# Kernel optimization log

Hardware: AMD Instinct MI355X
Metric: run time of the kernel (lower is better)

Reference implementation:

```python
import jax, jax.numpy as jnp
import numpy as np

MC = 16384
IND_T = 96
N_MAT = 4
N_STRIKES = 21


def _init_linear(key, fan_in, fan_out, prefix=()):
    k1, k2 = jax.random.split(key)
    lim = 1.0 / np.sqrt(fan_in)
    W = jax.random.uniform(k1, prefix + (fan_in, fan_out), minval=-lim, maxval=lim, dtype=jnp.float32)
    b = jax.random.uniform(k2, prefix + (fan_out,), minval=-lim, maxval=lim, dtype=jnp.float32)
    return W, b


def setup_inputs() -> dict:
    key = jax.random.key(0)
    ks = jax.random.split(key, 14)
    z = jax.random.normal(ks[0], (MC, IND_T), dtype=jnp.float32)
    zz = jax.random.normal(ks[1], (MC, IND_T), dtype=jnp.float32)
    timegrid = jnp.arange(IND_T + 1, dtype=jnp.float32) / 365.0  # daily grid
    maturities = jnp.array([24, 48, 72, 96], dtype=jnp.int32)    # in days
    strikes = jnp.linspace(0.8, 1.2, N_STRIKES, dtype=jnp.float32)
    sv_W1, sv_b1 = _init_linear(ks[2], 3, 100)
    sv_W2, sv_b2 = _init_linear(ks[3], 100, 100)
    sv_W3, sv_b3 = _init_linear(ks[4], 100, 1)
    vh_W1, vh_b1 = _init_linear(ks[5], 2, 20, (N_MAT,))
    vh_W2, vh_b2 = _init_linear(ks[6], 20, N_STRIKES, (N_MAT,))
    vd_W1, vd_b1 = _init_linear(ks[7], 1, 20)
    vd_W2, vd_b2 = _init_linear(ks[8], 20, 1)
    vv_W1, vv_b1 = _init_linear(ks[9], 1, 20)
    vv_W2, vv_b2 = _init_linear(ks[10], 20, 1)
    v0 = jax.random.uniform(ks[11], (1,), dtype=jnp.float32) * 0.1
    rho = jnp.ones((1,), dtype=jnp.float32) * -2.0
    return dict(S0=jnp.float32(1.0), rate=jnp.float32(0.05), z=z, zz=zz,
                timegrid=timegrid, strikes=strikes, v0=v0, rho=rho,
                sv_W1=sv_W1, sv_b1=sv_b1, sv_W2=sv_W2, sv_b2=sv_b2, sv_W3=sv_W3, sv_b3=sv_b3,
                vh_W1=vh_W1, vh_b1=vh_b1, vh_W2=vh_W2, vh_b2=vh_b2,
                vd_W1=vd_W1, vd_b1=vd_b1, vd_W2=vd_W2, vd_b2=vd_b2,
                vv_W1=vv_W1, vv_b1=vv_b1, vv_W2=vv_W2, vv_b2=vv_b2,
                maturities=maturities)


def reference(S0, rate, z, zz, timegrid, strikes, v0, rho,
              sv_W1, sv_b1, sv_W2, sv_b2, sv_W3, sv_b3,
              vh_W1, vh_b1, vh_W2, vh_b2,
              vd_W1, vd_b1, vd_W2, vd_b2,
              vv_W1, vv_b1, vv_W2, vv_b2,
              maturities):
    sg = jax.lax.stop_gradient
    mc = z.shape[0]
    n_mat = vh_W1.shape[0]
    n_strikes = strikes.shape[0]

    def s_vol(x):  # [MC,3] -> [MC,1], softplus output
        h1 = jax.nn.relu(x @ sv_W1 + sv_b1)
        h2 = jax.nn.relu(h1 @ sv_W2 + sv_b2)
        return jax.nn.softplus(h2 @ sv_W3 + sv_b3)

    def v_drift(v):  # [MC,1] -> [MC,1]
        return jax.nn.relu(v @ vd_W1 + vd_b1) @ vd_W2 + vd_b2

    def v_vol(v):  # [MC,1] -> [MC,1], softplus output
        return jax.nn.softplus(jax.nn.relu(v @ vv_W1 + vv_b1) @ vv_W2 + vv_b2)

    def vanilla_hedge_all(x):  # [MC,2] -> [MC, n_strikes, n_mat] (one net per maturity)
        h1 = jax.nn.relu(jnp.einsum('mi,kio->kmo', x, vh_W1) + vh_b1[:, None, :])
        out = jax.nn.softplus(jnp.einsum('kmo,koj->kmj', h1, vh_W2) + vh_b2[:, None, :])
        return jnp.transpose(out, (1, 2, 0))

    rho_t = jnp.tanh(rho)[0]
    days = jnp.round(timegrid * 365.0).astype(jnp.int32)       # [IND_T+1]
    le = days[1:, None] <= maturities[None, :]                  # [IND_T, n_mat]
    idx_net = jnp.argmax(le, axis=1)                            # first live maturity per step
    is_mat = jnp.any(days[1:, None] == maturities[None, :], axis=1)
    mat_idx = jnp.arange(n_mat)

    Slog0 = jnp.log(jnp.full((mc, 1), S0, dtype=jnp.float32))
    V0 = jnp.full((mc, 1), 1.0, dtype=jnp.float32) * jax.nn.sigmoid(v0)[0] * 0.5
    cv0 = jnp.zeros((mc, n_strikes, n_mat), dtype=jnp.float32)
    pv0 = jnp.zeros((n_mat, n_strikes), dtype=jnp.float32)

    xs = (z.T[:, :, None], zz.T[:, :, None], timegrid[:-1], timegrid[1:], idx_net, is_mat)

    def step(carry, x):
        Slog_old, V_old, cv, pv_h, pv_var = carry
        z_i, zz_i, t0, t1, idx, im = x
        h = t1 - t0
        sqh = jnp.sqrt(h)
        dW = sqh * z_i                                          # [MC,1]
        dB = rho_t * dW + jnp.sqrt(1.0 - rho_t ** 2) * sqh * zz_i
        ones_t = jnp.full((mc, 1), 1.0, dtype=jnp.float32) * t0
        pd = s_vol(jnp.concatenate([ones_t, Slog_old, V_old], axis=1))  # price diffusion
        cv_fwd = vanilla_hedge_all(jnp.concatenate([ones_t, sg(Slog_old)], axis=1))
        V_new = V_old + v_drift(V_old) * h + v_vol(V_old) * dB
        drift = rate - 0.5 * pd ** 2
        diff = pd * dW
        drift_c = 1.0 + jnp.abs(sg(drift)) * sqh                # tamed Euler
        diff_c = 1.0 + jnp.abs(sg(pd)) * sqh
        Slog_new = Slog_old + drift * h / drift_c + diff / diff_c
        S_new = jnp.exp(Slog_new)
        S_old = jnp.exp(Slog_old)
        dS = jnp.exp(-rate * t1) * S_new - jnp.exp(-rate * t0) * S_old  # [MC,1]
        mask = (mat_idx >= idx).astype(cv.dtype)                # live maturities only
        cv = cv + mask[None, None, :] * cv_fwd * sg(dS)[:, :, None]
        # hedged vanilla (call) prices collected at maturity steps
        payoff = jnp.exp(-rate * t1) * jnp.maximum(S_new - strikes[None, :], 0.0)
        price = payoff - cv[:, :, idx]                          # [MC, n_strikes]
        pv = jnp.mean(price, axis=0)
        pvar = jnp.var(price, axis=0, ddof=1)
        sel = (mat_idx == idx)[:, None] & im
        pv_h = jnp.where(sel, pv[None, :], pv_h)
        pv_var = jnp.where(sel, pvar[None, :], pv_var)
        return (Slog_new, V_new, cv, pv_h, pv_var), None

    (_, _, _, pv_h, pv_var), _ = jax.lax.scan(step, (Slog0, V0, cv0, pv0, pv0), xs)
    return jnp.stack([pv_h, pv_var])  # [2, n_mat, n_strikes]
```

## Files before the change

kernel.cpp:

```cpp
#include <hip/hip_runtime.h>
#include <hip/hip_bf16.h>
#include <math.h>


#define MC      16384
#define NSTEP   96
#define BLOCK   512
#define NGROUP  512
#define NPAIR   84

typedef short bf16x8 __attribute__((ext_vector_type(8)));
typedef float f32x4  __attribute__((ext_vector_type(4)));

union U8 { uint4 u; bf16x8 v; };
union BF2U { __hip_bfloat162 b; unsigned u; };

__device__ __forceinline__ unsigned bf16rne(float x) {
    unsigned u = __float_as_uint(x);
    return (u + 0x7FFFu + ((u >> 16) & 1u)) >> 16;
}
__device__ __forceinline__ unsigned pk2(float lo, float hi) {
    BF2U t; t.b = __float22bfloat162_rn(make_float2(lo, hi));
    return t.u;
}
__device__ __forceinline__ float sp(float x) {
    return fmaxf(x, 0.f) + __logf(1.f + __expf(-fabsf(x)));
}

__global__ __launch_bounds__(BLOCK, 4)
void lsv_sim(const float* __restrict__ S0p,   const float* __restrict__ ratep,
             const float* __restrict__ z,     const float* __restrict__ zzg,
             const float* __restrict__ strikesg,
             const float* __restrict__ v0p,   const float* __restrict__ rhop,
             const float* __restrict__ svW1,  const float* __restrict__ svb1,
             const float* __restrict__ svW2,  const float* __restrict__ svb2,
             const float* __restrict__ svW3,  const float* __restrict__ svb3,
             const float* __restrict__ vhW1,  const float* __restrict__ vhb1,
             const float* __restrict__ vhW2,  const float* __restrict__ vhb2,
             const float* __restrict__ vdW1,  const float* __restrict__ vdb1,
             const float* __restrict__ vdW2,  const float* __restrict__ vdb2,
             const float* __restrict__ vvW1,  const float* __restrict__ vvb1,
             const float* __restrict__ vvW2,  const float* __restrict__ vvb2,
             const int*   __restrict__ mats,
             float* __restrict__ psum, float* __restrict__ psq)
{
    __shared__ __align__(16) unsigned short H1c[16 * 32 * 8];
    __shared__ __align__(16) float W1f[16 * 32];
    __shared__ __align__(16) float WH1f[16 * 32];
    __shared__ __align__(16) float B2T[128], W3T[128];
    __shared__ __align__(16) float RED[32 * 4];
    __shared__ float VDl[32], VVl[32];
    __shared__ float PSs[2][32], PSq[2][32];
    __shared__ __align__(16) float VW[128];
    __shared__ __align__(16) float4 STEP[NSTEP];
    __shared__ float D1T[NSTEP];
    __shared__ int   ITAB[NSTEP];
    __shared__ float ZT[32][97], ZZT[32][97];
    __shared__ float SLOG[32], VST[32], SST[32], SLOGP[32], DSP[32];
    __shared__ __align__(16) float CW1[2][128];
    __shared__ __align__(16) float CH[2][128];

    const int tid  = threadIdx.x;
    const int lane = tid & 63;
    const int w    = __builtin_amdgcn_readfirstlane(tid >> 6);
    const int quad = lane >> 4;
    const int col  = lane & 15;
    const int lp   = lane & 31;

    const int pt = w & 1;
    const int jg = w >> 1;
    const int hm = w >> 1;

    {
        const size_t gbase = (size_t)blockIdx.x * 32 * NSTEP;
        for (int e = tid; e < 32 * NSTEP; e += BLOCK) {
            const int p = e / NSTEP, ii = e - p * NSTEP;
            ZT[p][ii]  = z  [gbase + e];
            ZZT[p][ii] = zzg[gbase + e];
        }
    }
    for (int e = tid; e < 128; e += BLOCK) {
        float v = 0.f;
        if      (e < 20)             v = vdW1[e];
        else if (e < 40)             v = vdb1[e - 20];
        else if (e < 60)             v = vdW2[e - 40];
        else if (e >= 64 && e < 84)  v = vvW1[e - 64];
        else if (e >= 84 && e < 104) v = vvb1[e - 84];
        else if (e >= 104 && e < 124)v = vvW2[e - 104];
        else if (e == 124)           v = vdb2[0];
        else if (e == 125)           v = vvb2[0];
        VW[e] = v;
        B2T[e] = (e < 100) ? svb2[e] : 0.f;
        W3T[e] = (e < 100) ? svW3[e] : 0.f;
    }
    for (int e = tid; e < 512; e += BLOCK) {
        const int kc2 = e >> 5, r5 = e & 31, grp = r5 >> 3, kk = kc2 * 8 + (r5 & 7);
        float v = 0.f;
        if (kk < 100) v = (grp == 0) ? svW1[kk] : (grp == 1) ? svW1[100 + kk]
                        : (grp == 2) ? svW1[200 + kk] : svb1[kk];
        W1f[e] = v;
    }
    for (int e = tid; e < 512; e += BLOCK) {
        const int hq = e >> 5, r5 = e & 31, grp = r5 >> 3;
        const int hmm = hq >> 2, qq = hq & 3;
        const int j = qq * 8 + (r5 & 7);
        float v = 0.f;
        if (j < 20 && grp < 3)
            v = (grp == 0) ? vhW1[hmm * 40 + j] : (grp == 1) ? vhW1[hmm * 40 + 20 + j]
                                                : vhb1[hmm * 20 + j];
        WH1f[e] = v;
    }

    const float rate  = ratep[0];
    const float S0    = S0p[0];
    const float rho_t = tanhf(rhop[0]);
    const float srho  = sqrtf(1.f - rho_t * rho_t);
    const float b3    = svb3[0];

    if (tid < NSTEP) {
        const int i = tid;
        const float t0 = (float)i       * (1.f / 365.f);
        const float t1 = (float)(i + 1) * (1.f / 365.f);
        const float h  = t1 - t0;
        STEP[i] = make_float4(t0, h, sqrtf(h), __expf(-rate * t0));
        D1T[i]  = __expf(-rate * t1);
        const int day = i + 1;
        const int m0 = mats[0], m1 = mats[1], m2 = mats[2], m3 = mats[3];
        const int idx = (day > m0) + (day > m1) + (day > m2);
        const int mi  = (idx == 0) ? m0 : (idx == 1) ? m1 : (idx == 2) ? m2 : m3;
        ITAB[i] = idx | ((day == mi) ? 256 : 0);
    }

    bf16x8 Af[4][2];
#pragma unroll
    for (int c = 0; c < 4; c++)
#pragma unroll
        for (int t = 0; t < 2; t++) {
            U8 tt;
#pragma unroll
            for (int e2 = 0; e2 < 4; e2++) {
                const int k0 = 32 * c + 8 * quad + 2 * e2;
                const int j  = (2 * jg + t) * 16 + col;
                const float v0 = (k0     < 100 && j < 100) ? svW2[k0 * 100 + j]       : 0.f;
                const float v1 = (k0 + 1 < 100 && j < 100) ? svW2[(k0 + 1) * 100 + j] : 0.f;
                (&tt.u.x)[e2] = bf16rne(v0) | (bf16rne(v1) << 16);
            }
            Af[c][t] = tt.v;
        }
    bf16x8 Ah[2];
#pragma unroll
    for (int st = 0; st < 2; st++) {
        U8 tt;
#pragma unroll
        for (int e2 = 0; e2 < 4; e2++) {
            const int j0 = 8 * quad + 2 * e2, j1 = j0 + 1;
            const int s  = st * 16 + col;
            const float v0 = (j0 < 20 && s < 21) ? vhW2[hm * 420 + j0 * 21 + s] : 0.f;
            const float v1 = (j1 < 20 && s < 21) ? vhW2[hm * 420 + j1 * 21 + s] : 0.f;
            (&tt.u.x)[e2] = bf16rne(v0) | (bf16rne(v1) << 16);
        }
        Ah[st] = tt.v;
    }
    f32x4 c0h, c1h;
    float K0a[4], K1a[4];
#pragma unroll
    for (int r = 0; r < 4; r++) {
        const int s0 = quad * 4 + r, s1 = 16 + quad * 4 + r;
        c0h[r] = vhb2[hm * 21 + s0];
        K0a[r] = strikesg[s0];
        c1h[r] = (s1 < 21) ? vhb2[hm * 21 + s1] : 0.f;
        K1a[r] = (s1 < 21) ? strikesg[s1] : 1e30f;
    }

    float Slog = __logf(S0);
    float S    = __expf(Slog);
    float V    = (1.f / (1.f + __expf(-v0p[0]))) * 0.5f;
    f32x4 cv0 = {0.f, 0.f, 0.f, 0.f};
    f32x4 cv1 = {0.f, 0.f, 0.f, 0.f};

    const int path = pt * 16 + col;
    const int kc   = jg * 4 + quad;

    __syncthreads();

    if (tid < 128) {
        const float t00 = STEP[0].x;
        const int kk = tid;
        CW1[0][kk] = fmaf(t00, W1f[(kk >> 3) * 32 + (kk & 7)],
                               W1f[(kk >> 3) * 32 + 24 + (kk & 7)]);
    } else if (tid < 256) {
        const float t00 = STEP[0].x;
        const int e = tid - 128;
        CH[0][e] = fmaf(t00, WH1f[(e >> 3) * 32 + (e & 7)],
                             WH1f[(e >> 3) * 32 + 16 + (e & 7)]);
    }
    if (tid < 32) {
        SLOG[tid] = Slog;
        SST[tid]  = S;
        VST[tid]  = V;
    }

    __syncthreads();

    const int j0e = (2 * jg) * 16 + quad * 4;
    const float4 b2a = *reinterpret_cast<const float4*>(B2T + j0e);
    const float4 w3a = *reinterpret_cast<const float4*>(W3T + j0e);
    const float4 b2b = *reinterpret_cast<const float4*>(B2T + j0e + 16);
    const float4 w3b = *reinterpret_cast<const float4*>(W3T + j0e + 16);

    auto hedge_step = [&](int ip) {
        const int iv   = ITAB[ip];
        const int idxp = iv & 0xff;
        if (hm >= idxp) {
            const int hb = ip & 1;
            const float slp = SLOGP[path];
            U8 b;
#pragma unroll
            for (int hh = 0; hh < 2; hh++) {
                const float* Wp = WH1f + (hm * 4 + quad) * 32 + 8 + hh * 4;
                const float4 ws4 = *reinterpret_cast<const float4*>(Wp);
                const float4 ch4 = *reinterpret_cast<const float4*>(&CH[hb][(hm * 4 + quad) * 8 + hh * 4]);
                const float x0 = fmaxf(ch4.x + slp * ws4.x, 0.f);
                const float x1 = fmaxf(ch4.y + slp * ws4.y, 0.f);
                const float x2 = fmaxf(ch4.z + slp * ws4.z, 0.f);
                const float x3 = fmaxf(ch4.w + slp * ws4.w, 0.f);
                (&b.u.x)[2 * hh]     = pk2(x0, x1);
                (&b.u.x)[2 * hh + 1] = pk2(x2, x3);
            }
            const f32x4 D0 = __builtin_amdgcn_mfma_f32_16x16x32_bf16(Ah[0], b.v, c0h, 0, 0, 0);
            const f32x4 D1 = __builtin_amdgcn_mfma_f32_16x16x32_bf16(Ah[1], b.v, c1h, 0, 0, 0);
            const float dsP = DSP[path];
#pragma unroll
            for (int r = 0; r < 4; r++) {
                cv0[r] += sp(D0[r]) * dsP;
                cv1[r] += sp(D1[r]) * dsP;
            }
            if ((iv & 256) && hm == idxp) {
                const float Sp  = SST[path];
                const float d1p = D1T[ip];
                float p0[4], q0[4], p1[4], q1[4];
#pragma unroll
                for (int r = 0; r < 4; r++) {
                    p0[r] = d1p * fmaxf(Sp - K0a[r], 0.f) - cv0[r];
                    p1[r] = d1p * fmaxf(Sp - K1a[r], 0.f) - cv1[r];
                    q0[r] = p0[r] * p0[r];
                    q1[r] = p1[r] * p1[r];
                }
#pragma unroll
                for (int o = 1; o <= 8; o <<= 1) {
#pragma unroll
                    for (int r = 0; r < 4; r++) {
                        p0[r] += __shfl_xor(p0[r], o);
                        q0[r] += __shfl_xor(q0[r], o);
                        p1[r] += __shfl_xor(p1[r], o);
                        q1[r] += __shfl_xor(q1[r], o);
                    }
                }
                if (col == 0) {
#pragma unroll
                    for (int r = 0; r < 4; r++) {
                        const int s0 = quad * 4 + r, s1 = 16 + quad * 4 + r;
                        PSs[pt][s0] = p0[r];  PSq[pt][s0] = q0[r];
                        if (s1 < 21) { PSs[pt][s1] = p1[r];  PSq[pt][s1] = q1[r]; }
                    }
                }
            }
        }
    };

    auto ps_reduce = [&](int ip) {
        if (w == 0) {
            const int iv = ITAB[ip];
            if (iv & 256) {
                const int s = lane & 31;
                if (s < 21) {
                    const float* src = (lane >= 32) ? &PSq[0][0] : &PSs[0][0];
                    const float acc = src[s] + src[32 + s];
                    float* dst = (lane >= 32) ? psq : psum;
                    dst[((iv & 0xff) * 21 + s) * NGROUP + blockIdx.x] = acc;
                }
            }
        }
    };

    for (int i = 0; i < NSTEP; i++) {
        const int buf = i & 1;

        {
            const float slp = SLOG[path];
            const float vp  = VST[path];
            const float* Wp = W1f + kc * 32;
            uint4 o;
#pragma unroll
            for (int hh = 0; hh < 2; hh++) {
                const float4 b4 = *reinterpret_cast<const float4*>(Wp + 8 + hh * 4);
                const float4 c4 = *reinterpret_cast<const float4*>(Wp + 16 + hh * 4);
                const float4 cw = *reinterpret_cast<const float4*>(&CW1[buf][kc * 8 + hh * 4]);
                const float x0 = fmaxf(cw.x + slp * b4.x + vp * c4.x, 0.f);
                const float x1 = fmaxf(cw.y + slp * b4.y + vp * c4.y, 0.f);
                const float x2 = fmaxf(cw.z + slp * b4.z + vp * c4.z, 0.f);
                const float x3 = fmaxf(cw.w + slp * b4.w + vp * c4.w, 0.f);
                (&o.x)[2 * hh]     = pk2(x0, x1);
                (&o.x)[2 * hh + 1] = pk2(x2, x3);
            }
            *reinterpret_cast<uint4*>(H1c + (kc * 32 + path) * 8) = o;
        }
        if (i > 0) hedge_step(i - 1);
        if (w == 0) {
            const float Vp = VST[lp];
            const float* bw = VW + ((lane >= 32) ? 64 : 0);
            float a2 = 0.f;
#pragma unroll
            for (int q5 = 0; q5 < 5; q5++) {
                const float4 w1 = *reinterpret_cast<const float4*>(bw + 4 * q5);
                const float4 b1 = *reinterpret_cast<const float4*>(bw + 20 + 4 * q5);
                const float4 w2 = *reinterpret_cast<const float4*>(bw + 40 + 4 * q5);
                a2 += fmaxf(Vp * w1.x + b1.x, 0.f) * w2.x;
                a2 += fmaxf(Vp * w1.y + b1.y, 0.f) * w2.y;
                a2 += fmaxf(Vp * w1.z + b1.z, 0.f) * w2.z;
                a2 += fmaxf(Vp * w1.w + b1.w, 0.f) * w2.w;
            }
            if (lane < 32) VDl[lp] = a2; else VVl[lp] = a2;
        }
        __syncthreads();

        {
            f32x4 d0 = {0.f, 0.f, 0.f, 0.f};
            f32x4 d1 = {0.f, 0.f, 0.f, 0.f};
#pragma unroll
            for (int c = 0; c < 4; c++) {
                const bf16x8 b = *reinterpret_cast<const bf16x8*>(
                    H1c + ((quad + 4 * c) * 32 + path) * 8);
                d0 = __builtin_amdgcn_mfma_f32_16x16x32_bf16(Af[c][0], b, d0, 0, 0, 0);
                d1 = __builtin_amdgcn_mfma_f32_16x16x32_bf16(Af[c][1], b, d1, 0, 0, 0);
            }
            float acc = fmaxf(d0[0] + b2a.x, 0.f) * w3a.x
                      + fmaxf(d0[1] + b2a.y, 0.f) * w3a.y
                      + fmaxf(d0[2] + b2a.z, 0.f) * w3a.z
                      + fmaxf(d0[3] + b2a.w, 0.f) * w3a.w
                      + fmaxf(d1[0] + b2b.x, 0.f) * w3b.x
                      + fmaxf(d1[1] + b2b.y, 0.f) * w3b.y
                      + fmaxf(d1[2] + b2b.z, 0.f) * w3b.z
                      + fmaxf(d1[3] + b2b.w, 0.f) * w3b.w;
            acc += __shfl_xor(acc, 16);
            acc += __shfl_xor(acc, 32);
            if (quad == 0)
                RED[path * 4 + jg] = acc;
        }
        if (i > 0) ps_reduce(i - 1);
        __syncthreads();

        if (w == 1) {
            const float4 rr = *reinterpret_cast<const float4*>(RED + lp * 4);
            const float pout = (rr.x + rr.y) + (rr.z + rr.w);
            const float pd = sp(pout + b3);
            const float vdv = VDl[lp] + VW[124];
            const float vvv = sp(VVl[lp] + VW[125]);
            const float4 u  = STEP[i];
            const float sqh = u.z;
            const float zi  = ZT[lp][i];
            const float zzi = ZZT[lp][i];
            const float dW = sqh * zi;
            const float dB = rho_t * dW + srho * sqh * zzi;
            const float Vn = V + vdv * u.y + vvv * dB;
            const float drift   = rate - 0.5f * pd * pd;
            const float diff    = pd * dW;
            const float drift_c = 1.f + fabsf(drift) * sqh;
            const float diff_c  = 1.f + fabsf(pd) * sqh;
            const float Sln = Slog + __fdividef(drift * u.y, drift_c) + __fdividef(diff, diff_c);
            const float Sn  = __expf(Sln);
            const float dS  = D1T[i] * Sn - u.w * S;
            if (lane < 32) {
                SLOGP[lp] = Slog;  DSP[lp] = dS;
                SLOG[lp]  = Sln;   SST[lp] = Sn;  VST[lp] = Vn;
            }
            Slog = Sln; S = Sn; V = Vn;
        } else if ((w == 2 || w == 3) && i + 1 < NSTEP) {
            const float t0n = STEP[i + 1].x;
            const int kk = (w - 2) * 64 + lane;
            CW1[buf ^ 1][kk] = fmaf(t0n, W1f[(kk >> 3) * 32 + (kk & 7)],
                                         W1f[(kk >> 3) * 32 + 24 + (kk & 7)]);
        } else if ((w == 4 || w == 5) && i + 1 < NSTEP) {
            const float t0n = STEP[i + 1].x;
            const int e = (w - 4) * 64 + lane;
            CH[buf ^ 1][e] = fmaf(t0n, WH1f[(e >> 3) * 32 + (e & 7)],
                                       WH1f[(e >> 3) * 32 + 16 + (e & 7)]);
        }
        __syncthreads();
    }

    hedge_step(NSTEP - 1);
    __syncthreads();
    ps_reduce(NSTEP - 1);
}

__global__ void lsv_finalize(const float* __restrict__ psum,
                             const float* __restrict__ psq,
                             float* __restrict__ out)
{
    const int t    = blockIdx.x;
    const int lane = threadIdx.x;
    float s = 0.f, q = 0.f;
    for (int b = lane; b < NGROUP; b += 64) {
        s += psum[t * NGROUP + b];
        q += psq [t * NGROUP + b];
    }
#pragma unroll
    for (int o = 1; o <= 32; o <<= 1) {
        s += __shfl_xor(s, o);
        q += __shfl_xor(q, o);
    }
    if (lane == 0) {
        const float mean = s * (1.0f / (float)MC);
        const float var  = (q - (float)MC * mean * mean) * (1.0f / (float)(MC - 1));
        out[t]         = mean;
        out[NPAIR + t] = var;
    }
}

extern "C" void kernel_launch(void* const* d_in, const int* in_sizes, int n_in,
                              void* d_out, int out_size, void* d_ws, size_t ws_size,
                              hipStream_t stream)
{
    const float* S0    = (const float*)d_in[0];
    const float* rate  = (const float*)d_in[1];
    const float* z     = (const float*)d_in[2];
    const float* zz    = (const float*)d_in[3];
    const float* strikes = (const float*)d_in[5];
    const float* v0    = (const float*)d_in[6];
    const float* rho   = (const float*)d_in[7];
    const float* svW1  = (const float*)d_in[8];
    const float* svb1  = (const float*)d_in[9];
    const float* svW2  = (const float*)d_in[10];
    const float* svb2  = (const float*)d_in[11];
    const float* svW3  = (const float*)d_in[12];
    const float* svb3  = (const float*)d_in[13];
    const float* vhW1  = (const float*)d_in[14];
    const float* vhb1  = (const float*)d_in[15];
    const float* vhW2  = (const float*)d_in[16];
    const float* vhb2  = (const float*)d_in[17];
    const float* vdW1  = (const float*)d_in[18];
    const float* vdb1  = (const float*)d_in[19];
    const float* vdW2  = (const float*)d_in[20];
    const float* vdb2  = (const float*)d_in[21];
    const float* vvW1  = (const float*)d_in[22];
    const float* vvb1  = (const float*)d_in[23];
    const float* vvW2  = (const float*)d_in[24];
    const float* vvb2  = (const float*)d_in[25];
    const int*   mats  = (const int*)d_in[26];

    float* psum = (float*)d_ws;
    float* psq  = psum + NPAIR * NGROUP;

    hipLaunchKernelGGL(lsv_sim, dim3(NGROUP), dim3(BLOCK), 0, stream,
                       S0, rate, z, zz, strikes, v0, rho,
                       svW1, svb1, svW2, svb2, svW3, svb3,
                       vhW1, vhb1, vhW2, vhb2,
                       vdW1, vdb1, vdW2, vdb2,
                       vvW1, vvb1, vvW2, vvb2,
                       mats, psum, psq);

    hipLaunchKernelGGL(lsv_finalize, dim3(NPAIR), dim3(64), 0, stream,
                       psum, psq, (float*)d_out);
}
```

Measured before the change: 392.3 us.

## Interleave two path groups per block to overlap serial SDE update with MFMA work

Each block now simulates two independent 32-path groups (64 paths) instead of one, and the grid is halved. Within each time step the groups are staggered: one group's serial SDE update (r3) and hedge/variance work run while the other group's layer-1 and MFMA layers execute. This hides the single-wave serial update and leaves fewer idle waves between barriers, with three barriers per step covering both groups. In exchange it doubles the LDS footprint and per-thread accumulators, lowers the launch_bounds occupancy target from 4 to 2, and reduces the number of blocks, so there is less parallelism across the GPU.

Result: slower. 407.3 us (+3.8%).

```diff
diff --git a/kernel.cpp b/kernel.cpp
--- a/kernel.cpp
+++ b/kernel.cpp
@@ -6,6 +6,7 @@
 #define MC      16384
 #define NSTEP   96
 #define BLOCK   512
+#define GRID    256
 #define NGROUP  512
 #define NPAIR   84
 
@@ -27,7 +28,7 @@
     return fmaxf(x, 0.f) + __logf(1.f + __expf(-fabsf(x)));
 }
 
-__global__ __launch_bounds__(BLOCK, 4)
+__global__ __launch_bounds__(BLOCK, 2)
 void lsv_sim(const float* __restrict__ S0p,   const float* __restrict__ ratep,
              const float* __restrict__ z,     const float* __restrict__ zzg,
              const float* __restrict__ strikesg,
@@ -44,19 +45,19 @@
              const int*   __restrict__ mats,
              float* __restrict__ psum, float* __restrict__ psq)
 {
-    __shared__ __align__(16) unsigned short H1c[16 * 32 * 8];
+    __shared__ __align__(16) unsigned short H1c[2][16 * 32 * 8];
     __shared__ __align__(16) float W1f[16 * 32];
     __shared__ __align__(16) float WH1f[16 * 32];
     __shared__ __align__(16) float B2T[128], W3T[128];
-    __shared__ __align__(16) float RED[32 * 4];
-    __shared__ float VDl[32], VVl[32];
-    __shared__ float PSs[2][32], PSq[2][32];
+    __shared__ __align__(16) float RED[2][32 * 4];
+    __shared__ float VDb[2][2][32], VVb[2][2][32];
+    __shared__ float PSs[2][2][32], PSq[2][2][32];
     __shared__ __align__(16) float VW[128];
     __shared__ __align__(16) float4 STEP[NSTEP];
     __shared__ float D1T[NSTEP];
     __shared__ int   ITAB[NSTEP];
-    __shared__ float ZT[32][97], ZZT[32][97];
-    __shared__ float SLOG[32], VST[32], SST[32], SLOGP[32], DSP[32];
+    __shared__ float ZT[64][97], ZZT[64][97];
+    __shared__ float SLOG[2][32], VST[2][32], SST[2][32], SLOGP[2][32], DSP[2][32];
     __shared__ __align__(16) float CW1[2][128];
     __shared__ __align__(16) float CH[2][128];
 
@@ -70,10 +71,12 @@
     const int pt = w & 1;
     const int jg = w >> 1;
     const int hm = w >> 1;
+    const int pl = pt * 16 + col;
+    const int kc = jg * 4 + quad;
 
     {
-        const size_t gbase = (size_t)blockIdx.x * 32 * NSTEP;
-        for (int e = tid; e < 32 * NSTEP; e += BLOCK) {
+        const size_t gbase = (size_t)blockIdx.x * 64 * NSTEP;
+        for (int e = tid; e < 64 * NSTEP; e += BLOCK) {
             const int p = e / NSTEP, ii = e - p * NSTEP;
             ZT[p][ii]  = z  [gbase + e];
             ZZT[p][ii] = zzg[gbase + e];
@@ -172,14 +175,8 @@
         K1a[r] = (s1 < 21) ? strikesg[s1] : 1e30f;
     }
 
-    float Slog = __logf(S0);
-    float S    = __expf(Slog);
-    float V    = (1.f / (1.f + __expf(-v0p[0]))) * 0.5f;
-    f32x4 cv0 = {0.f, 0.f, 0.f, 0.f};
-    f32x4 cv1 = {0.f, 0.f, 0.f, 0.f};
-
-    const int path = pt * 16 + col;
-    const int kc   = jg * 4 + quad;
+    f32x4 cv0A = {0.f,0.f,0.f,0.f}, cv1A = {0.f,0.f,0.f,0.f};
+    f32x4 cv0B = {0.f,0.f,0.f,0.f}, cv1B = {0.f,0.f,0.f,0.f};
 
     __syncthreads();
 
@@ -194,10 +191,12 @@
         CH[0][e] = fmaf(t00, WH1f[(e >> 3) * 32 + (e & 7)],
                              WH1f[(e >> 3) * 32 + 16 + (e & 7)]);
     }
-    if (tid < 32) {
-        SLOG[tid] = Slog;
-        SST[tid]  = S;
-        VST[tid]  = V;
+    if (tid < 64) {
+        const int g = tid >> 5, p = tid & 31;
+        const float Slog0 = __logf(S0);
+        SLOG[g][p] = Slog0;
+        SST[g][p]  = __expf(Slog0);
+        VST[g][p]  = (1.f / (1.f + __expf(-v0p[0]))) * 0.5f;
     }
 
     __syncthreads();
@@ -207,36 +206,60 @@
     const float4 w3a = *reinterpret_cast<const float4*>(W3T + j0e);
     const float4 b2b = *reinterpret_cast<const float4*>(B2T + j0e + 16);
     const float4 w3b = *reinterpret_cast<const float4*>(W3T + j0e + 16);
-
-    auto hedge_step = [&](int ip) {
+    const float4 wsA = *reinterpret_cast<const float4*>(WH1f + (hm * 4 + quad) * 32 + 8);
+    const float4 wsB = *reinterpret_cast<const float4*>(WH1f + (hm * 4 + quad) * 32 + 12);
+
+    auto p1_step = [&](int g, int buf) {
+        const float slp = SLOG[g][pl];
+        const float vp  = VST[g][pl];
+        const float* Wp = W1f + kc * 32;
+        uint4 o;
+#pragma unroll
+        for (int hh = 0; hh < 2; hh++) {
+            const float4 b4 = *reinterpret_cast<const float4*>(Wp + 8 + hh * 4);
+            const float4 c4 = *reinterpret_cast<const float4*>(Wp + 16 + hh * 4);
+            const float4 cw = *reinterpret_cast<const float4*>(&CW1[buf][kc * 8 + hh * 4]);
+            const float x0 = fmaxf(cw.x + slp * b4.x + vp * c4.x, 0.f);
+            const float x1 = fmaxf(cw.y + slp * b4.y + vp * c4.y, 0.f);
+            const float x2 = fmaxf(cw.z + slp * b4.z + vp * c4.z, 0.f);
+            const float x3 = fmaxf(cw.w + slp * b4.w + vp * c4.w, 0.f);
+            (&o.x)[2 * hh]     = pk2(x0, x1);
+            (&o.x)[2 * hh + 1] = pk2(x2, x3);
+        }
+        *reinterpret_cast<uint4*>(&H1c[g][(kc * 32 + pl) * 8]) = o;
+    };
+
+    auto hedge_step = [&](int g, int ip, f32x4& cv0, f32x4& cv1) {
         const int iv   = ITAB[ip];
         const int idxp = iv & 0xff;
         if (hm >= idxp) {
             const int hb = ip & 1;
-            const float slp = SLOGP[path];
+            const float slp = SLOGP[g][pl];
             U8 b;
-#pragma unroll
-            for (int hh = 0; hh < 2; hh++) {
-                const float* Wp = WH1f + (hm * 4 + quad) * 32 + 8 + hh * 4;
-                const float4 ws4 = *reinterpret_cast<const float4*>(Wp);
-                const float4 ch4 = *reinterpret_cast<const float4*>(&CH[hb][(hm * 4 + quad) * 8 + hh * 4]);
-                const float x0 = fmaxf(ch4.x + slp * ws4.x, 0.f);
-                const float x1 = fmaxf(ch4.y + slp * ws4.y, 0.f);
-                const float x2 = fmaxf(ch4.z + slp * ws4.z, 0.f);
-                const float x3 = fmaxf(ch4.w + slp * ws4.w, 0.f);
-                (&b.u.x)[2 * hh]     = pk2(x0, x1);
-                (&b.u.x)[2 * hh + 1] = pk2(x2, x3);
+            {
+                const float4 ch4 = *reinterpret_cast<const float4*>(&CH[hb][(hm * 4 + quad) * 8]);
+                (&b.u.x)[0] = pk2(fmaxf(ch4.x + slp * wsA.x, 0.f),
+                                  fmaxf(ch4.y + slp * wsA.y, 0.f));
+                (&b.u.x)[1] = pk2(fmaxf(ch4.z + slp * wsA.z, 0.f),
+                                  fmaxf(ch4.w + slp * wsA.w, 0.f));
+            }
+            {
+                const float4 ch4 = *reinterpret_cast<const float4*>(&CH[hb][(hm * 4 + quad) * 8 + 4]);
+                (&b.u.x)[2] = pk2(fmaxf(ch4.x + slp * wsB.x, 0.f),
+                                  fmaxf(ch4.y + slp * wsB.y, 0.f));
+                (&b.u.x)[3] = pk2(fmaxf(ch4.z + slp * wsB.z, 0.f),
+                                  fmaxf(ch4.w + slp * wsB.w, 0.f));
             }
             const f32x4 D0 = __builtin_amdgcn_mfma_f32_16x16x32_bf16(Ah[0], b.v, c0h, 0, 0, 0);
             const f32x4 D1 = __builtin_amdgcn_mfma_f32_16x16x32_bf16(Ah[1], b.v, c1h, 0, 0, 0);
-            const float dsP = DSP[path];
+            const float dsP = DSP[g][pl];
 #pragma unroll
             for (int r = 0; r < 4; r++) {
                 cv0[r] += sp(D0[r]) * dsP;
                 cv1[r] += sp(D1[r]) * dsP;
             }
             if ((iv & 256) && hm == idxp) {
-                const float Sp  = SST[path];
+                const float Sp  = SST[g][pl];
                 const float d1p = D1T[ip];
                 float p0[4], q0[4], p1[4], q1[4];
 #pragma unroll
@@ -260,24 +283,96 @@
 #pragma unroll
                     for (int r = 0; r < 4; r++) {
                         const int s0 = quad * 4 + r, s1 = 16 + quad * 4 + r;
-                        PSs[pt][s0] = p0[r];  PSq[pt][s0] = q0[r];
-                        if (s1 < 21) { PSs[pt][s1] = p1[r];  PSq[pt][s1] = q1[r]; }
+                        PSs[g][pt][s0] = p0[r];  PSq[g][pt][s0] = q0[r];
+                        if (s1 < 21) { PSs[g][pt][s1] = p1[r];  PSq[g][pt][s1] = q1[r]; }
                     }
                 }
             }
         }
     };
 
-    auto ps_reduce = [&](int ip) {
+    auto mfma_main = [&](int g) {
+        f32x4 d0 = {0.f,0.f,0.f,0.f};
+        f32x4 d1 = {0.f,0.f,0.f,0.f};
+#pragma unroll
+        for (int c = 0; c < 4; c++) {
+            const bf16x8 b = *reinterpret_cast<const bf16x8*>(
+                &H1c[g][((quad + 4 * c) * 32 + pl) * 8]);
+            d0 = __builtin_amdgcn_mfma_f32_16x16x32_bf16(Af[c][0], b, d0, 0, 0, 0);
+            d1 = __builtin_amdgcn_mfma_f32_16x16x32_bf16(Af[c][1], b, d1, 0, 0, 0);
+        }
+        float acc = fmaxf(d0[0] + b2a.x, 0.f) * w3a.x
+                  + fmaxf(d0[1] + b2a.y, 0.f) * w3a.y
+                  + fmaxf(d0[2] + b2a.z, 0.f) * w3a.z
+                  + fmaxf(d0[3] + b2a.w, 0.f) * w3a.w
+                  + fmaxf(d1[0] + b2b.x, 0.f) * w3b.x
+                  + fmaxf(d1[1] + b2b.y, 0.f) * w3b.y
+                  + fmaxf(d1[2] + b2b.z, 0.f) * w3b.z
+                  + fmaxf(d1[3] + b2b.w, 0.f) * w3b.w;
+        acc += __shfl_xor(acc, 16);
+        acc += __shfl_xor(acc, 32);
+        if (quad == 0)
+            RED[g][pl * 4 + jg] = acc;
+    };
+
+    auto r3 = [&](int g, int i) {
+        if (w == 1) {
+            const float4 rr = *reinterpret_cast<const float4*>(&RED[g][lp * 4]);
+            const float pout = (rr.x + rr.y) + (rr.z + rr.w);
+            const float pd  = sp(pout + b3);
+            const float vdv = VDb[g][i & 1][lp] + VW[124];
+            const float vvv = sp(VVb[g][i & 1][lp] + VW[125]);
+            const float4 u  = STEP[i];
+            const float sqh = u.z;
+            const float zi  = ZT[g * 32 + lp][i];
+            const float zzi = ZZT[g * 32 + lp][i];
+            const float dW = sqh * zi;
+            const float dB = rho_t * dW + srho * sqh * zzi;
+            const float Vold  = VST[g][lp];
+            const float Sold  = SST[g][lp];
+            const float SlogO = SLOG[g][lp];
+            const float Vn = Vold + vdv * u.y + vvv * dB;
+            const float drift   = rate - 0.5f * pd * pd;
+            const float diff    = pd * dW;
+            const float drift_c = 1.f + fabsf(drift) * sqh;
+            const float diff_c  = 1.f + fabsf(pd) * sqh;
+            const float Sln = SlogO + __fdividef(drift * u.y, drift_c) + __fdividef(diff, diff_c);
+            const float Sn  = __expf(Sln);
+            const float dS  = D1T[i] * Sn - u.w * Sold;
+            if (lane < 32) {
+                SLOGP[g][lp] = SlogO;  DSP[g][lp] = dS;
+                SLOG[g][lp]  = Sln;    SST[g][lp] = Sn;  VST[g][lp] = Vn;
+            }
+        }
+    };
+
+    auto vnets = [&](int g, int buf) {
+        const float Vp = VST[g][lp];
+        const float* bw = VW + ((lane >= 32) ? 64 : 0);
+        float a2 = 0.f;
+#pragma unroll
+        for (int q5 = 0; q5 < 5; q5++) {
+            const float4 w1 = *reinterpret_cast<const float4*>(bw + 4 * q5);
+            const float4 b1 = *reinterpret_cast<const float4*>(bw + 20 + 4 * q5);
+            const float4 w2 = *reinterpret_cast<const float4*>(bw + 40 + 4 * q5);
+            a2 += fmaxf(Vp * w1.x + b1.x, 0.f) * w2.x;
+            a2 += fmaxf(Vp * w1.y + b1.y, 0.f) * w2.y;
+            a2 += fmaxf(Vp * w1.z + b1.z, 0.f) * w2.z;
+            a2 += fmaxf(Vp * w1.w + b1.w, 0.f) * w2.w;
+        }
+        if (lane < 32) VDb[g][buf][lp] = a2; else VVb[g][buf][lp] = a2;
+    };
+
+    auto ps_reduce = [&](int g, int ip) {
         if (w == 0) {
             const int iv = ITAB[ip];
             if (iv & 256) {
                 const int s = lane & 31;
                 if (s < 21) {
-                    const float* src = (lane >= 32) ? &PSq[0][0] : &PSs[0][0];
+                    const float* src = (lane >= 32) ? &PSq[g][0][0] : &PSs[g][0][0];
                     const float acc = src[s] + src[32 + s];
                     float* dst = (lane >= 32) ? psq : psum;
-                    dst[((iv & 0xff) * 21 + s) * NGROUP + blockIdx.x] = acc;
+                    dst[((iv & 0xff) * 21 + s) * NGROUP + blockIdx.x * 2 + g] = acc;
                 }
             }
         }
@@ -286,96 +381,26 @@
     for (int i = 0; i < NSTEP; i++) {
         const int buf = i & 1;
 
-        {
-            const float slp = SLOG[path];
-            const float vp  = VST[path];
-            const float* Wp = W1f + kc * 32;
-            uint4 o;
-#pragma unroll
-            for (int hh = 0; hh < 2; hh++) {
-                const float4 b4 = *reinterpret_cast<const float4*>(Wp + 8 + hh * 4);
-                const float4 c4 = *reinterpret_cast<const float4*>(Wp + 16 + hh * 4);
-                const float4 cw = *reinterpret_cast<const float4*>(&CW1[buf][kc * 8 + hh * 4]);
-                const float x0 = fmaxf(cw.x + slp * b4.x + vp * c4.x, 0.f);
-                const float x1 = fmaxf(cw.y + slp * b4.y + vp * c4.y, 0.f);
-                const float x2 = fmaxf(cw.z + slp * b4.z + vp * c4.z, 0.f);
-                const float x3 = fmaxf(cw.w + slp * b4.w + vp * c4.w, 0.f);
-                (&o.x)[2 * hh]     = pk2(x0, x1);
-                (&o.x)[2 * hh + 1] = pk2(x2, x3);
-            }
-            *reinterpret_cast<uint4*>(H1c + (kc * 32 + path) * 8) = o;
-        }
-        if (i > 0) hedge_step(i - 1);
-        if (w == 0) {
-            const float Vp = VST[lp];
-            const float* bw = VW + ((lane >= 32) ? 64 : 0);
-            float a2 = 0.f;
-#pragma unroll
-            for (int q5 = 0; q5 < 5; q5++) {
-                const float4 w1 = *reinterpret_cast<const float4*>(bw + 4 * q5);
-                const float4 b1 = *reinterpret_cast<const float4*>(bw + 20 + 4 * q5);
-                const float4 w2 = *reinterpret_cast<const float4*>(bw + 40 + 4 * q5);
-                a2 += fmaxf(Vp * w1.x + b1.x, 0.f) * w2.x;
-                a2 += fmaxf(Vp * w1.y + b1.y, 0.f) * w2.y;
-                a2 += fmaxf(Vp * w1.z + b1.z, 0.f) * w2.z;
-                a2 += fmaxf(Vp * w1.w + b1.w, 0.f) * w2.w;
-            }
-            if (lane < 32) VDl[lp] = a2; else VVl[lp] = a2;
-        }
+        p1_step(0, buf);
+        if (i > 0) {
+            hedge_step(0, i - 1, cv0A, cv1A);
+            r3(1, i - 1);
+        }
+        if (w == 0) vnets(0, buf);
         __syncthreads();
 
-        {
-            f32x4 d0 = {0.f, 0.f, 0.f, 0.f};
-            f32x4 d1 = {0.f, 0.f, 0.f, 0.f};
-#pragma unroll
-            for (int c = 0; c < 4; c++) {
-                const bf16x8 b = *reinterpret_cast<const bf16x8*>(
-                    H1c + ((quad + 4 * c) * 32 + path) * 8);
-                d0 = __builtin_amdgcn_mfma_f32_16x16x32_bf16(Af[c][0], b, d0, 0, 0, 0);
-                d1 = __builtin_amdgcn_mfma_f32_16x16x32_bf16(Af[c][1], b, d1, 0, 0, 0);
-            }
-            float acc = fmaxf(d0[0] + b2a.x, 0.f) * w3a.x
-                      + fmaxf(d0[1] + b2a.y, 0.f) * w3a.y
-                      + fmaxf(d0[2] + b2a.z, 0.f) * w3a.z
-                      + fmaxf(d0[3] + b2a.w, 0.f) * w3a.w
-                      + fmaxf(d1[0] + b2b.x, 0.f) * w3b.x
-                      + fmaxf(d1[1] + b2b.y, 0.f) * w3b.y
-                      + fmaxf(d1[2] + b2b.z, 0.f) * w3b.z
-                      + fmaxf(d1[3] + b2b.w, 0.f) * w3b.w;
-            acc += __shfl_xor(acc, 16);
-            acc += __shfl_xor(acc, 32);
-            if (quad == 0)
-                RED[path * 4 + jg] = acc;
-        }
-        if (i > 0) ps_reduce(i - 1);
+        mfma_main(0);
+        p1_step(1, buf);
+        if (i > 0) {
+            hedge_step(1, i - 1, cv0B, cv1B);
+            ps_reduce(0, i - 1);
+        }
+        if (w == 1) vnets(1, buf);
         __syncthreads();
 
-        if (w == 1) {
-            const float4 rr = *reinterpret_cast<const float4*>(RED + lp * 4);
-            const float pout = (rr.x + rr.y) + (rr.z + rr.w);
-            const float pd = sp(pout + b3);
-            const float vdv = VDl[lp] + VW[124];
-            const float vvv = sp(VVl[lp] + VW[125]);
-            const float4 u  = STEP[i];
-            const float sqh = u.z;
-            const float zi  = ZT[lp][i];
-            const float zzi = ZZT[lp][i];
-            const float dW = sqh * zi;
-            const float dB = rho_t * dW + srho * sqh * zzi;
-            const float Vn = V + vdv * u.y + vvv * dB;
-            const float drift   = rate - 0.5f * pd * pd;
-            const float diff    = pd * dW;
-            const float drift_c = 1.f + fabsf(drift) * sqh;
-            const float diff_c  = 1.f + fabsf(pd) * sqh;
-            const float Sln = Slog + __fdividef(drift * u.y, drift_c) + __fdividef(diff, diff_c);
-            const float Sn  = __expf(Sln);
-            const float dS  = D1T[i] * Sn - u.w * S;
-            if (lane < 32) {
-                SLOGP[lp] = Slog;  DSP[lp] = dS;
-                SLOG[lp]  = Sln;   SST[lp] = Sn;  VST[lp] = Vn;
-            }
-            Slog = Sln; S = Sn; V = Vn;
-        } else if ((w == 2 || w == 3) && i + 1 < NSTEP) {
+        mfma_main(1);
+        r3(0, i);
+        if ((w == 2 || w == 3) && i + 1 < NSTEP) {
             const float t0n = STEP[i + 1].x;
             const int kk = (w - 2) * 64 + lane;
             CW1[buf ^ 1][kk] = fmaf(t0n, W1f[(kk >> 3) * 32 + (kk & 7)],
@@ -386,12 +411,17 @@
             CH[buf ^ 1][e] = fmaf(t0n, WH1f[(e >> 3) * 32 + (e & 7)],
                                        WH1f[(e >> 3) * 32 + 16 + (e & 7)]);
         }
+        if (i > 0) ps_reduce(1, i - 1);
         __syncthreads();
     }
 
-    hedge_step(NSTEP - 1);
+    hedge_step(0, NSTEP - 1, cv0A, cv1A);
+    r3(1, NSTEP - 1);
     __syncthreads();
-    ps_reduce(NSTEP - 1);
+    ps_reduce(0, NSTEP - 1);
+    hedge_step(1, NSTEP - 1, cv0B, cv1B);
+    __syncthreads();
+    ps_reduce(1, NSTEP - 1);
 }
 
 __global__ void lsv_finalize(const float* __restrict__ psum,
@@ -452,7 +482,7 @@
     float* psum = (float*)d_ws;
     float* psq  = psum + NPAIR * NGROUP;
 
-    hipLaunchKernelGGL(lsv_sim, dim3(NGROUP), dim3(BLOCK), 0, stream,
+    hipLaunchKernelGGL(lsv_sim, dim3(GRID), dim3(BLOCK), 0, stream,
                        S0, rate, z, zz, strikes, v0, rho,
                        svW1, svb1, svW2, svb2, svW3, svb3,
                        vhW1, vhb1, vhW2, vhb2,
```
